# Kernel optimization log

Hardware: AMD Instinct MI355X
Metric: run time of the kernel (lower is better)

## Reference

```python
import jax, jax.numpy as jnp
import numpy as np

B, H, S, D = 4, 16, 2048, 64

def setup_inputs() -> dict:
    key = jax.random.key(0)
    kq, kk, kv = jax.random.split(key, 3)
    q = jax.random.normal(kq, (B, H, S, D), dtype=jnp.float32)
    k = jax.random.normal(kk, (B, H, S, D), dtype=jnp.float32)
    v = jax.random.normal(kv, (B, H, S, D), dtype=jnp.float32)
    # broadcastable causal mask: True = attend
    mask = jnp.tril(jnp.ones((S, S), dtype=bool))[None, None, :, :]
    return {"q": q, "k": k, "v": v, "mask": mask}

def reference(q, k, v, mask):
    # qk = einsum('... q d, ... k d -> ... q k'); mask -> -inf; softmax(qk/sqrt(d_k)); @ v
    scale = 1.0 / jnp.sqrt(jnp.asarray(q.shape[-1], q.dtype))
    scores = jnp.einsum('bhqd,bhkd->bhqk', q, k)
    scores = jnp.where(mask, scores, -jnp.inf) * scale  # -inf * scale stays -inf
    attn = jax.nn.softmax(scores, axis=-1)
    return jnp.einsum('bhqk,bhkd->bhqd', attn, v)
```

## Files before the change

### kernel.cpp

```cpp
#include <hip/hip_runtime.h>


#define SEQ 2048
#define HD  64

typedef __attribute__((ext_vector_type(8))) short short8;
typedef __attribute__((ext_vector_type(4))) float f32x4;

__device__ __forceinline__ unsigned f2bfu(float f) {
    union { float f; unsigned u; } x; x.f = f;
    return (x.u + 0x7fff + ((x.u >> 16) & 1)) >> 16;
}
__device__ __forceinline__ unsigned pk2(float lo, float hi) {
    return f2bfu(lo) | (f2bfu(hi) << 16);
}

__global__ __launch_bounds__(256, 2) void sdpa_kernel(
    const float* __restrict__ Q, const float* __restrict__ K,
    const float* __restrict__ V, float* __restrict__ O)
{
    __shared__ __align__(16) char smraw[16384];
    char* Kl = smraw;
    char* Vl = smraw + 8192;

    const int bx = blockIdx.x;
    const int qt = 15 - (bx >> 6);
    const int bh = bx & 63;
    const int qbase = qt * 128;

    const int tid  = threadIdx.x;
    const int lane = tid & 63;
    const int w    = tid >> 6;
    const int g    = lane >> 4;
    const int r16  = lane & 15;
    const int wq   = qbase + w * 32;

    const size_t base = (size_t)bh * (SEQ * HD);

    const float SC = 0.18033688011112042f;
    short8 qf[2][2];
    #pragma unroll
    for (int qs = 0; qs < 2; ++qs) {
        const float* qp = Q + base + (size_t)(wq + qs * 16 + r16) * HD + 8 * g;
        #pragma unroll
        for (int c = 0; c < 2; ++c) {
            f32x4 a = *(const f32x4*)(qp + c * 32);
            f32x4 b = *(const f32x4*)(qp + c * 32 + 4);
            union { short8 s; unsigned u[4]; } t;
            t.u[0] = pk2(a[0] * SC, a[1] * SC);
            t.u[1] = pk2(a[2] * SC, a[3] * SC);
            t.u[2] = pk2(b[0] * SC, b[1] * SC);
            t.u[3] = pk2(b[2] * SC, b[3] * SC);
            qf[qs][c] = t.s;
        }
    }

    f32x4 oacc[2][4] = {};
    float mrun[2] = {-1e30f, -1e30f};
    float lrun[2] = {0.0f, 0.0f};

    const int k_kvo = tid >> 2;
    const int k_o   = k_kvo & 31;
    const int k_row = (k_kvo & 32) + 16 * ((k_o >> 2) & 1) + 4 * (k_o >> 3) + (k_o & 3);
    const int k_dc  = (tid & 3) * 2;
    const int v_kv0 = (tid & 31) * 2;
    const int v_db  = (tid >> 5) * 8;

    const int nkvb = (qbase + 128) >> 6;
    for (int kvb = 0; kvb < nkvb; ++kvb) {
        const int kvbase = kvb << 6;

        {
            const float* kp = K + base + (size_t)(kvbase + k_kvo) * HD + k_dc * 8;
            f32x4 a0 = *(const f32x4*)(kp + 0);
            f32x4 a1 = *(const f32x4*)(kp + 4);
            f32x4 b0 = *(const f32x4*)(kp + 8);
            f32x4 b1 = *(const f32x4*)(kp + 12);
            union { short8 s; unsigned u[4]; } c0, c1;
            c0.u[0] = pk2(a0[0], a0[1]); c0.u[1] = pk2(a0[2], a0[3]);
            c0.u[2] = pk2(a1[0], a1[1]); c0.u[3] = pk2(a1[2], a1[3]);
            c1.u[0] = pk2(b0[0], b0[1]); c1.u[1] = pk2(b0[2], b0[3]);
            c1.u[2] = pk2(b1[0], b1[1]); c1.u[3] = pk2(b1[2], b1[3]);
            const int r7 = k_row & 7;
            *(short8*)(Kl + ((k_row * 8 + (k_dc ^ r7)) << 4))       = c0.s;
            *(short8*)(Kl + ((k_row * 8 + ((k_dc + 1) ^ r7)) << 4)) = c1.s;
        }
        {
            const float* vp = V + base + (size_t)(kvbase + v_kv0) * HD + v_db;
            f32x4 a0 = *(const f32x4*)(vp + 0);
            f32x4 a1 = *(const f32x4*)(vp + 4);
            f32x4 b0 = *(const f32x4*)(vp + HD);
            f32x4 b1 = *(const f32x4*)(vp + HD + 4);
            const int u  = v_kv0 >> 3;
            const int wo = (v_kv0 & 7) * 2;
            #pragma unroll
            for (int i = 0; i < 4; ++i) {
                const int d = v_db + i;
                *(unsigned*)(Vl + ((d * 8 + (u ^ (d & 7))) << 4) + wo) = pk2(a0[i], b0[i]);
            }
            #pragma unroll
            for (int i = 0; i < 4; ++i) {
                const int d = v_db + 4 + i;
                *(unsigned*)(Vl + ((d * 8 + (u ^ (d & 7))) << 4) + wo) = pk2(a1[i], b1[i]);
            }
        }
        __syncthreads();

        if (kvbase <= wq + 31) {
            f32x4 sa[2][2][2];
            #pragma unroll
            for (int qs = 0; qs < 2; ++qs)
                #pragma unroll
                for (int c2 = 0; c2 < 2; ++c2)
                    #pragma unroll
                    for (int t = 0; t < 2; ++t)
                        sa[qs][c2][t] = (f32x4){0.f, 0.f, 0.f, 0.f};
            #pragma unroll
            for (int c2 = 0; c2 < 2; ++c2)
                #pragma unroll
                for (int t = 0; t < 2; ++t)
                    #pragma unroll
                    for (int c = 0; c < 2; ++c) {
                        const int row = c2 * 32 + t * 16 + r16;
                        short8 kf = *(const short8*)(Kl + ((row * 8 + ((4 * c + g) ^ (row & 7))) << 4));
                        sa[0][c2][t] = __builtin_amdgcn_mfma_f32_16x16x32_bf16(kf, qf[0][c], sa[0][c2][t], 0, 0, 0);
                        sa[1][c2][t] = __builtin_amdgcn_mfma_f32_16x16x32_bf16(kf, qf[1][c], sa[1][c2][t], 0, 0, 0);
                    }

            #pragma unroll
            for (int qs = 0; qs < 2; ++qs) {
                const int q0 = wq + qs * 16;
                const int qrow = q0 + r16;
                if (kvbase + 63 > q0) {
                    #pragma unroll
                    for (int c2 = 0; c2 < 2; ++c2)
                        #pragma unroll
                        for (int t = 0; t < 2; ++t)
                            #pragma unroll
                            for (int r = 0; r < 4; ++r) {
                                const int kv = kvbase + c2 * 32 + 8 * g + 4 * t + r;
                                if (kv > qrow) sa[qs][c2][t][r] = -1e30f;
                            }
                }
                float mloc = sa[qs][0][0][0];
                #pragma unroll
                for (int c2 = 0; c2 < 2; ++c2)
                    #pragma unroll
                    for (int t = 0; t < 2; ++t)
                        #pragma unroll
                        for (int r = 0; r < 4; ++r)
                            mloc = fmaxf(mloc, sa[qs][c2][t][r]);
                mloc = fmaxf(mloc, __shfl_xor(mloc, 16));
                mloc = fmaxf(mloc, __shfl_xor(mloc, 32));
                const float mnew  = fmaxf(mrun[qs], mloc);
                const float alpha = __builtin_amdgcn_exp2f(mrun[qs] - mnew);
                float ls = 0.0f;
                #pragma unroll
                for (int c2 = 0; c2 < 2; ++c2)
                    #pragma unroll
                    for (int t = 0; t < 2; ++t)
                        #pragma unroll
                        for (int r = 0; r < 4; ++r) {
                            const float p = __builtin_amdgcn_exp2f(sa[qs][c2][t][r] - mnew);
                            sa[qs][c2][t][r] = p;
                            ls += p;
                        }
                ls += __shfl_xor(ls, 16);
                ls += __shfl_xor(ls, 32);
                lrun[qs] = lrun[qs] * alpha + ls;
                mrun[qs] = mnew;
                #pragma unroll
                for (int dt = 0; dt < 4; ++dt) oacc[qs][dt] *= alpha;
            }

            #pragma unroll
            for (int c2 = 0; c2 < 2; ++c2) {
                union { short8 s; unsigned u[4]; } pf0, pf1;
                pf0.u[0] = pk2(sa[0][c2][0][0], sa[0][c2][0][1]);
                pf0.u[1] = pk2(sa[0][c2][0][2], sa[0][c2][0][3]);
                pf0.u[2] = pk2(sa[0][c2][1][0], sa[0][c2][1][1]);
                pf0.u[3] = pk2(sa[0][c2][1][2], sa[0][c2][1][3]);
                pf1.u[0] = pk2(sa[1][c2][0][0], sa[1][c2][0][1]);
                pf1.u[1] = pk2(sa[1][c2][0][2], sa[1][c2][0][3]);
                pf1.u[2] = pk2(sa[1][c2][1][0], sa[1][c2][1][1]);
                pf1.u[3] = pk2(sa[1][c2][1][2], sa[1][c2][1][3]);
                #pragma unroll
                for (int dt = 0; dt < 4; ++dt) {
                    const int row = dt * 16 + r16;
                    short8 vf = *(const short8*)(Vl + ((row * 8 + ((c2 * 4 + g) ^ (row & 7))) << 4));
                    oacc[0][dt] = __builtin_amdgcn_mfma_f32_16x16x32_bf16(vf, pf0.s, oacc[0][dt], 0, 0, 0);
                    oacc[1][dt] = __builtin_amdgcn_mfma_f32_16x16x32_bf16(vf, pf1.s, oacc[1][dt], 0, 0, 0);
                }
            }
        }
        __syncthreads();
    }

    #pragma unroll
    for (int qs = 0; qs < 2; ++qs) {
        const float inv = 1.0f / lrun[qs];
        float* op = O + base + (size_t)(wq + qs * 16 + r16) * HD + 4 * g;
        #pragma unroll
        for (int dt = 0; dt < 4; ++dt) {
            f32x4 vv = oacc[qs][dt] * inv;
            *(f32x4*)(op + dt * 16) = vv;
        }
    }
}

extern "C" void kernel_launch(void* const* d_in, const int* in_sizes, int n_in,
                              void* d_out, int out_size, void* d_ws, size_t ws_size,
                              hipStream_t stream) {
    (void)in_sizes; (void)n_in; (void)out_size; (void)d_ws; (void)ws_size;
    const float* q = (const float*)d_in[0];
    const float* k = (const float*)d_in[1];
    const float* v = (const float*)d_in[2];
    float* o = (float*)d_out;
    sdpa_kernel<<<dim3(64 * 16), dim3(256), 0, stream>>>(q, k, v, o);
}
```

Measured before the change: 224.0 us.

## Double-buffer K/V tiles with register prefetch and lazy softmax rescaling

```diff
diff --git a/kernel.cpp b/kernel.cpp
--- a/kernel.cpp
+++ b/kernel.cpp
@@ -19,9 +19,7 @@
     const float* __restrict__ Q, const float* __restrict__ K,
     const float* __restrict__ V, float* __restrict__ O)
 {
-    __shared__ __align__(16) char smraw[16384];
-    char* Kl = smraw;
-    char* Vl = smraw + 8192;
+    __shared__ __align__(16) char smraw[32768];
 
     const int bx = blockIdx.x;
     const int qt = 15 - (bx >> 6);
@@ -66,47 +64,62 @@
     const int v_kv0 = (tid & 31) * 2;
     const int v_db  = (tid >> 5) * 8;
 
+    f32x4 ka0, ka1, kb0, kb1, va0, va1, vb0, vb1;
+
+    auto LOADT = [&](int kvbase) {
+        const float* kp = K + base + (size_t)(kvbase + k_kvo) * HD + k_dc * 8;
+        ka0 = *(const f32x4*)(kp + 0);
+        ka1 = *(const f32x4*)(kp + 4);
+        kb0 = *(const f32x4*)(kp + 8);
+        kb1 = *(const f32x4*)(kp + 12);
+        const float* vp = V + base + (size_t)(kvbase + v_kv0) * HD + v_db;
+        va0 = *(const f32x4*)(vp + 0);
+        va1 = *(const f32x4*)(vp + 4);
+        vb0 = *(const f32x4*)(vp + HD);
+        vb1 = *(const f32x4*)(vp + HD + 4);
+    };
+    auto WRITET = [&](int b) {
+        char* Kl = smraw + b * 16384;
+        char* Vl = Kl + 8192;
+        union { short8 s; unsigned u[4]; } c0, c1;
+        c0.u[0] = pk2(ka0[0], ka0[1]); c0.u[1] = pk2(ka0[2], ka0[3]);
+        c0.u[2] = pk2(ka1[0], ka1[1]); c0.u[3] = pk2(ka1[2], ka1[3]);
+        c1.u[0] = pk2(kb0[0], kb0[1]); c1.u[1] = pk2(kb0[2], kb0[3]);
+        c1.u[2] = pk2(kb1[0], kb1[1]); c1.u[3] = pk2(kb1[2], kb1[3]);
+        const int r7 = k_row & 7;
+        *(short8*)(Kl + ((k_row * 8 + (k_dc ^ r7)) << 4))       = c0.s;
+        *(short8*)(Kl + ((k_row * 8 + ((k_dc + 1) ^ r7)) << 4)) = c1.s;
+        const int u  = v_kv0 >> 3;
+        const int wo = (v_kv0 & 7) * 2;
+        #pragma unroll
+        for (int i = 0; i < 4; ++i) {
+            const int d = v_db + i;
+            *(unsigned*)(Vl + ((d * 8 + (u ^ (d & 7))) << 4) + wo) = pk2(va0[i], vb0[i]);
+        }
+        #pragma unroll
+        for (int i = 0; i < 4; ++i) {
+            const int d = v_db + 4 + i;
+            *(unsigned*)(Vl + ((d * 8 + (u ^ (d & 7))) << 4) + wo) = pk2(va1[i], vb1[i]);
+        }
+    };
+
     const int nkvb = (qbase + 128) >> 6;
+
+    LOADT(0);
+    WRITET(0);
+    __syncthreads();
+
     for (int kvb = 0; kvb < nkvb; ++kvb) {
         const int kvbase = kvb << 6;
-
-        {
-            const float* kp = K + base + (size_t)(kvbase + k_kvo) * HD + k_dc * 8;
-            f32x4 a0 = *(const f32x4*)(kp + 0);
-            f32x4 a1 = *(const f32x4*)(kp + 4);
-            f32x4 b0 = *(const f32x4*)(kp + 8);
-            f32x4 b1 = *(const f32x4*)(kp + 12);
-            union { short8 s; unsigned u[4]; } c0, c1;
-            c0.u[0] = pk2(a0[0], a0[1]); c0.u[1] = pk2(a0[2], a0[3]);
-            c0.u[2] = pk2(a1[0], a1[1]); c0.u[3] = pk2(a1[2], a1[3]);
-            c1.u[0] = pk2(b0[0], b0[1]); c1.u[1] = pk2(b0[2], b0[3]);
-            c1.u[2] = pk2(b1[0], b1[1]); c1.u[3] = pk2(b1[2], b1[3]);
-            const int r7 = k_row & 7;
-            *(short8*)(Kl + ((k_row * 8 + (k_dc ^ r7)) << 4))       = c0.s;
-            *(short8*)(Kl + ((k_row * 8 + ((k_dc + 1) ^ r7)) << 4)) = c1.s;
-        }
-        {
-            const float* vp = V + base + (size_t)(kvbase + v_kv0) * HD + v_db;
-            f32x4 a0 = *(const f32x4*)(vp + 0);
-            f32x4 a1 = *(const f32x4*)(vp + 4);
-            f32x4 b0 = *(const f32x4*)(vp + HD);
-            f32x4 b1 = *(const f32x4*)(vp + HD + 4);
-            const int u  = v_kv0 >> 3;
-            const int wo = (v_kv0 & 7) * 2;
-            #pragma unroll
-            for (int i = 0; i < 4; ++i) {
-                const int d = v_db + i;
-                *(unsigned*)(Vl + ((d * 8 + (u ^ (d & 7))) << 4) + wo) = pk2(a0[i], b0[i]);
-            }
-            #pragma unroll
-            for (int i = 0; i < 4; ++i) {
-                const int d = v_db + 4 + i;
-                *(unsigned*)(Vl + ((d * 8 + (u ^ (d & 7))) << 4) + wo) = pk2(a1[i], b1[i]);
-            }
-        }
-        __syncthreads();
+        const int buf = kvb & 1;
+        const bool more = (kvb + 1 < nkvb);
+
+        if (more) LOADT((kvb + 1) << 6);
 
         if (kvbase <= wq + 31) {
+            const char* Kl = smraw + buf * 16384;
+            const char* Vl = Kl + 8192;
+
             f32x4 sa[2][2][2];
             #pragma unroll
             for (int qs = 0; qs < 2; ++qs)
@@ -115,6 +128,7 @@
                     #pragma unroll
                     for (int t = 0; t < 2; ++t)
                         sa[qs][c2][t] = (f32x4){0.f, 0.f, 0.f, 0.f};
+            __builtin_amdgcn_s_setprio(1);
             #pragma unroll
             for (int c2 = 0; c2 < 2; ++c2)
                 #pragma unroll
@@ -126,12 +140,13 @@
                         sa[0][c2][t] = __builtin_amdgcn_mfma_f32_16x16x32_bf16(kf, qf[0][c], sa[0][c2][t], 0, 0, 0);
                         sa[1][c2][t] = __builtin_amdgcn_mfma_f32_16x16x32_bf16(kf, qf[1][c], sa[1][c2][t], 0, 0, 0);
                     }
+            __builtin_amdgcn_s_setprio(0);
 
             #pragma unroll
             for (int qs = 0; qs < 2; ++qs) {
                 const int q0 = wq + qs * 16;
-                const int qrow = q0 + r16;
                 if (kvbase + 63 > q0) {
+                    const int qrow = q0 + r16;
                     #pragma unroll
                     for (int c2 = 0; c2 < 2; ++c2)
                         #pragma unroll
@@ -142,6 +157,11 @@
                                 if (kv > qrow) sa[qs][c2][t][r] = -1e30f;
                             }
                 }
+            }
+
+            float mnew[2];
+            #pragma unroll
+            for (int qs = 0; qs < 2; ++qs) {
                 float mloc = sa[qs][0][0][0];
                 #pragma unroll
                 for (int c2 = 0; c2 < 2; ++c2)
@@ -152,8 +172,20 @@
                             mloc = fmaxf(mloc, sa[qs][c2][t][r]);
                 mloc = fmaxf(mloc, __shfl_xor(mloc, 16));
                 mloc = fmaxf(mloc, __shfl_xor(mloc, 32));
-                const float mnew  = fmaxf(mrun[qs], mloc);
-                const float alpha = __builtin_amdgcn_exp2f(mrun[qs] - mnew);
+                mnew[qs] = fmaxf(mrun[qs], mloc);
+            }
+            if (!__all((mnew[0] - mrun[0] <= 8.0f) && (mnew[1] - mrun[1] <= 8.0f))) {
+                #pragma unroll
+                for (int qs = 0; qs < 2; ++qs) {
+                    const float alpha = __builtin_amdgcn_exp2f(mrun[qs] - mnew[qs]);
+                    lrun[qs] *= alpha;
+                    mrun[qs] = mnew[qs];
+                    #pragma unroll
+                    for (int dt = 0; dt < 4; ++dt) oacc[qs][dt] *= alpha;
+                }
+            }
+            #pragma unroll
+            for (int qs = 0; qs < 2; ++qs) {
                 float ls = 0.0f;
                 #pragma unroll
                 for (int c2 = 0; c2 < 2; ++c2)
@@ -161,16 +193,13 @@
                     for (int t = 0; t < 2; ++t)
                         #pragma unroll
                         for (int r = 0; r < 4; ++r) {
-                            const float p = __builtin_amdgcn_exp2f(sa[qs][c2][t][r] - mnew);
+                            const float p = __builtin_amdgcn_exp2f(sa[qs][c2][t][r] - mrun[qs]);
                             sa[qs][c2][t][r] = p;
                             ls += p;
                         }
                 ls += __shfl_xor(ls, 16);
                 ls += __shfl_xor(ls, 32);
-                lrun[qs] = lrun[qs] * alpha + ls;
-                mrun[qs] = mnew;
-                #pragma unroll
-                for (int dt = 0; dt < 4; ++dt) oacc[qs][dt] *= alpha;
+                lrun[qs] += ls;
             }
 
             #pragma unroll
@@ -184,6 +213,7 @@
                 pf1.u[1] = pk2(sa[1][c2][0][2], sa[1][c2][0][3]);
                 pf1.u[2] = pk2(sa[1][c2][1][0], sa[1][c2][1][1]);
                 pf1.u[3] = pk2(sa[1][c2][1][2], sa[1][c2][1][3]);
+                __builtin_amdgcn_s_setprio(1);
                 #pragma unroll
                 for (int dt = 0; dt < 4; ++dt) {
                     const int row = dt * 16 + r16;
@@ -191,9 +221,14 @@
                     oacc[0][dt] = __builtin_amdgcn_mfma_f32_16x16x32_bf16(vf, pf0.s, oacc[0][dt], 0, 0, 0);
                     oacc[1][dt] = __builtin_amdgcn_mfma_f32_16x16x32_bf16(vf, pf1.s, oacc[1][dt], 0, 0, 0);
                 }
-            }
-        }
-        __syncthreads();
+                __builtin_amdgcn_s_setprio(0);
+            }
+        }
+
+        if (more) {
+            WRITET(buf ^ 1);
+            __syncthreads();
+        }
     }
 
     #pragma unroll
```

Result: faster. 202.2 us (-9.7%).
